# Performance work log

Hardware: AMD Instinct MI355X
Metric: run time of the kernel (lower is better)

Reference implementation:

```python
import jax, jax.numpy as jnp
import numpy as np

HEADS = 2
NEG_SLOPE = 0.2  # PyG GATConv default leaky_relu slope


def gat_conv(x, edge_index, W, a_src, a_dst, bias, num_nodes):
    """PyG-style GATConv with concat=True and self-loops.
    x: [N, Fin], W: [Fin, H*C], a_src/a_dst: [H, C], bias: [H*C].
    edge_index: [2, E] with row 0 = source j, row 1 = target i.
    """
    H = HEADS
    C = W.shape[1] // H
    # add self loops
    loops = jnp.arange(num_nodes, dtype=edge_index.dtype)
    src = jnp.concatenate([edge_index[0], loops])
    dst = jnp.concatenate([edge_index[1], loops])

    xW = (x @ W).reshape(num_nodes, H, C)            # [N, H, C]
    alpha_s = jnp.einsum('nhc,hc->nh', xW, a_src)    # [N, H]
    alpha_d = jnp.einsum('nhc,hc->nh', xW, a_dst)    # [N, H]
    e = alpha_s[src] + alpha_d[dst]                  # [E, H]
    e = jax.nn.leaky_relu(e, NEG_SLOPE)
    # segment softmax over edges sharing the same target node
    m = jax.ops.segment_max(e, dst, num_segments=num_nodes)  # [N, H]
    e = jnp.exp(e - m[dst])
    denom = jax.ops.segment_sum(e, dst, num_segments=num_nodes)  # [N, H]
    alpha = e / denom[dst]                           # [E, H]
    # message = alpha_ij * xW_j, aggregated at target i
    msg = xW[src] * alpha[:, :, None]                # [E, H, C]
    out = jax.ops.segment_sum(msg, dst, num_segments=num_nodes)  # [N, H, C]
    return out.reshape(num_nodes, H * C) + bias


def setup_inputs() -> dict:
    key = jax.random.key(0)
    ks = jax.random.split(key, 10)
    N, E = 50000, 800000
    Fin, D = 128, 128
    H = HEADS
    x = jax.random.normal(ks[0], (N, Fin), dtype=jnp.float32)
    edge_index = jax.random.randint(ks[1], (2, E), 0, N, dtype=jnp.int64)
    g = 1.0 / np.sqrt(Fin)
    W1 = jax.random.normal(ks[2], (Fin, H * D), dtype=jnp.float32) * g
    a_src1 = jax.random.normal(ks[3], (H, D), dtype=jnp.float32) * g
    a_dst1 = jax.random.normal(ks[4], (H, D), dtype=jnp.float32) * g
    b1 = jnp.zeros((H * D,), dtype=jnp.float32)
    g2 = 1.0 / np.sqrt(H * D)
    W2 = jax.random.normal(ks[5], (H * D, H * D), dtype=jnp.float32) * g2
    a_src2 = jax.random.normal(ks[6], (H, D), dtype=jnp.float32) * g2
    a_dst2 = jax.random.normal(ks[7], (H, D), dtype=jnp.float32) * g2
    b2 = jnp.zeros((H * D,), dtype=jnp.float32)
    return {"x": x, "edge_index": edge_index,
            "W1": W1, "a_src1": a_src1, "a_dst1": a_dst1, "b1": b1,
            "W2": W2, "a_src2": a_src2, "a_dst2": a_dst2, "b2": b2}


def reference(x, edge_index, W1, a_src1, a_dst1, b1, W2, a_src2, a_dst2, b2):
    N = x.shape[0]
    h = gat_conv(x, edge_index, W1, a_src1, a_dst1, b1, N)
    h = jax.nn.elu(h)
    # dropout is identity in eval mode (deterministic reference)
    out = gat_conv(h, edge_index, W2, a_src2, a_dst2, b2, N)
    return out
```

## Files before the change

kernel.cpp:

```cpp
#include <hip/hip_runtime.h>
#include <math.h>

#define HEADS 2
#define CH    128
#define HC    256
#define NEG   0.2f

typedef __attribute__((ext_vector_type(8))) _Float16 half8;
typedef __attribute__((ext_vector_type(4))) float    f32x4;

__device__ inline unsigned short f2h(float x) {
    _Float16 h = (_Float16)x;
    unsigned short u;
    __builtin_memcpy(&u, &h, 2);
    return u;
}

__global__ __launch_bounds__(256)
void wcast_kernel(const float* __restrict__ W, unsigned short* __restrict__ Wt, int K) {
    const int idx = blockIdx.x * 256 + threadIdx.x;
    if (idx >= K * HC) return;
    const int k = idx >> 8;
    const int n = idx & 255;
    Wt[(size_t)n * K + k] = f2h(W[idx]);
}

__global__ __launch_bounds__(256)
void va_kernel(const float* __restrict__ W, const float* __restrict__ a_src,
               const float* __restrict__ a_dst, float* __restrict__ va, int K) {
    const int k    = (blockIdx.x * 256 + threadIdx.x) >> 6;
    const int lane = threadIdx.x & 63;
    if (k >= K) return;
    const int c0 = lane * 4;
    const float4 w4 = *reinterpret_cast<const float4*>(&W[(size_t)k * HC + c0]);
    const float4 s4 = *reinterpret_cast<const float4*>(&a_src[c0]);
    const float4 d4 = *reinterpret_cast<const float4*>(&a_dst[c0]);
    float ps = w4.x * s4.x + w4.y * s4.y + w4.z * s4.z + w4.w * s4.w;
    float pd = w4.x * d4.x + w4.y * d4.y + w4.z * d4.z + w4.w * d4.w;
    #pragma unroll
    for (int m = 1; m <= 16; m <<= 1) {
        ps += __shfl_xor(ps, m);
        pd += __shfl_xor(pd, m);
    }
    if (lane == 0)  { va[k * 4 + 0] = ps; va[k * 4 + 2] = pd; }
    if (lane == 32) { va[k * 4 + 1] = ps; va[k * 4 + 3] = pd; }
}

__global__ __launch_bounds__(256)
void xprep_kernel(const float* __restrict__ x, const float* __restrict__ va,
                  unsigned short* __restrict__ xb, float* __restrict__ as_out,
                  float* __restrict__ ad_out, int N, int K) {
    const int i    = (blockIdx.x * 256 + threadIdx.x) >> 6;
    const int lane = threadIdx.x & 63;
    if (i >= N) return;
    const float2 v = reinterpret_cast<const float2*>(&x[(size_t)i * K])[lane];
    ushort2 bv; bv.x = f2h(v.x); bv.y = f2h(v.y);
    reinterpret_cast<ushort2*>(&xb[(size_t)i * K])[lane] = bv;

    const float4 a0 = reinterpret_cast<const float4*>(va)[lane * 2 + 0];
    const float4 a1 = reinterpret_cast<const float4*>(va)[lane * 2 + 1];
    float p0 = v.x * a0.x + v.y * a1.x;
    float p1 = v.x * a0.y + v.y * a1.y;
    float p2 = v.x * a0.z + v.y * a1.z;
    float p3 = v.x * a0.w + v.y * a1.w;
    #pragma unroll
    for (int m = 1; m <= 32; m <<= 1) {
        p0 += __shfl_xor(p0, m);
        p1 += __shfl_xor(p1, m);
        p2 += __shfl_xor(p2, m);
        p3 += __shfl_xor(p3, m);
    }
    if (lane == 0) {
        as_out[i * 2 + 0] = p0; as_out[i * 2 + 1] = p1;
        ad_out[i * 2 + 0] = p2; ad_out[i * 2 + 1] = p3;
    }
}

__global__ __launch_bounds__(256)
void gemm_msg_kernel(const unsigned short* __restrict__ Ab,
                     const unsigned short* __restrict__ Wt,
                     unsigned short* __restrict__ xWh, int M, int K) {
    __shared__ unsigned short Ah[128][40];
    __shared__ unsigned short Bh[128][40];

    const int t    = threadIdx.x;
    const int row0 = blockIdx.x * 128;
    const int col0 = blockIdx.y * 128;
    const int lane = t & 63;
    const int wid  = t >> 6;
    const int wr   = wid >> 1;
    const int wc   = wid & 1;

    f32x4 acc[4][4] = {};

    const int arow = t & 127;
    const int aseg = (t >> 7) * 16;

    for (int kk = 0; kk < K; kk += 32) {
        {
            const int gr = row0 + arow;
            half8 v0 = {0,0,0,0,0,0,0,0}, v1 = {0,0,0,0,0,0,0,0};
            if (gr < M) {
                v0 = *reinterpret_cast<const half8*>(&Ab[(size_t)gr * K + kk + aseg]);
                v1 = *reinterpret_cast<const half8*>(&Ab[(size_t)gr * K + kk + aseg + 8]);
            }
            *reinterpret_cast<half8*>(&Ah[arow][aseg])     = v0;
            *reinterpret_cast<half8*>(&Ah[arow][aseg + 8]) = v1;
            const half8 w0 = *reinterpret_cast<const half8*>(
                &Wt[(size_t)(col0 + arow) * K + kk + aseg]);
            const half8 w1 = *reinterpret_cast<const half8*>(
                &Wt[(size_t)(col0 + arow) * K + kk + aseg + 8]);
            *reinterpret_cast<half8*>(&Bh[arow][aseg])     = w0;
            *reinterpret_cast<half8*>(&Bh[arow][aseg + 8]) = w1;
        }
        __syncthreads();

        half8 ah[4], bh[4];
        const int ko = (lane >> 4) * 8;
        #pragma unroll
        for (int m = 0; m < 4; ++m)
            ah[m] = *reinterpret_cast<const half8*>(&Ah[wr * 64 + m * 16 + (lane & 15)][ko]);
        #pragma unroll
        for (int n = 0; n < 4; ++n)
            bh[n] = *reinterpret_cast<const half8*>(&Bh[wc * 64 + n * 16 + (lane & 15)][ko]);

        #pragma unroll
        for (int m = 0; m < 4; ++m)
            #pragma unroll
            for (int n = 0; n < 4; ++n)
                acc[m][n] = __builtin_amdgcn_mfma_f32_16x16x32_f16(ah[m], bh[n], acc[m][n], 0, 0, 0);
        __syncthreads();
    }

    #pragma unroll
    for (int m = 0; m < 4; ++m) {
        #pragma unroll
        for (int reg = 0; reg < 4; ++reg) {
            const int gr = row0 + wr * 64 + m * 16 + (lane >> 4) * 4 + reg;
            if (gr < M) {
                unsigned short* rp = &xWh[(size_t)gr * HC + col0];
                #pragma unroll
                for (int n = 0; n < 4; ++n)
                    rp[wc * 64 + n * 16 + (lane & 15)] = f2h(acc[m][n][reg]);
            }
        }
    }
}

__global__ __launch_bounds__(256)
void hist_kernel(const int* __restrict__ dst, int* __restrict__ counts, int E) {
    const int e = blockIdx.x * 256 + threadIdx.x;
    if (e < E) atomicAdd(&counts[dst[e]], 1);
}

__global__ __launch_bounds__(256)
void scan_local_kernel(int* __restrict__ data, int* __restrict__ chunk_sum, int N) {
    __shared__ int s[256];
    const int t   = threadIdx.x;
    const int idx = blockIdx.x * 256 + t;
    const int v   = (idx < N) ? data[idx] : 0;
    s[t] = v;
    __syncthreads();
    #pragma unroll
    for (int off = 1; off < 256; off <<= 1) {
        int x = (t >= off) ? s[t - off] : 0;
        __syncthreads();
        s[t] += x;
        __syncthreads();
    }
    if (idx < N) data[idx] = s[t] - v;
    if (t == 255) chunk_sum[blockIdx.x] = s[255];
}

__global__ __launch_bounds__(256)
void scan_chunks_kernel(int* __restrict__ chunk, int nb) {
    __shared__ int s[256];
    const int t = threadIdx.x;
    const int v = (t < nb) ? chunk[t] : 0;
    s[t] = v;
    __syncthreads();
    #pragma unroll
    for (int off = 1; off < 256; off <<= 1) {
        int x = (t >= off) ? s[t - off] : 0;
        __syncthreads();
        s[t] += x;
        __syncthreads();
    }
    if (t < nb) chunk[t] = s[t] - v;
}

__global__ __launch_bounds__(256)
void add_offsets_kernel(const int* __restrict__ excl, const int* __restrict__ chunk_excl,
                        int* __restrict__ row_ptr, int* __restrict__ cursor,
                        int N, int E) {
    const int idx = blockIdx.x * 256 + threadIdx.x;
    if (idx < N) {
        const int rp = excl[idx] + chunk_excl[idx >> 8];
        row_ptr[idx] = rp;
        cursor[idx]  = rp;
    }
    if (idx == 0) row_ptr[N] = E;
}

__global__ __launch_bounds__(256)
void scatter_kernel(const int* __restrict__ src, const int* __restrict__ dst,
                    int* __restrict__ cursor, int* __restrict__ col_idx, int E) {
    const int e = blockIdx.x * 256 + threadIdx.x;
    if (e < E) {
        const int pos = atomicAdd(&cursor[dst[e]], 1);
        col_idx[pos] = src[e];
    }
}

__global__ __launch_bounds__(256)
void agg_kernel(const int* __restrict__ row_ptr, const int* __restrict__ col_idx,
                const unsigned short* __restrict__ xWh,
                const float* __restrict__ as_, const float* __restrict__ ad_,
                const float* __restrict__ bias, float* __restrict__ outf,
                unsigned short* __restrict__ hb, const float* __restrict__ va,
                float* __restrict__ as2, float* __restrict__ ad2,
                int N, int mode) {
    const int wv   = (blockIdx.x * 256 + threadIdx.x) >> 6;
    const int lane = threadIdx.x & 63;
    if (wv >= N) return;
    const int i    = wv;
    const int half = lane >> 5;
    const int sl   = lane & 31;
    const int hh   = sl >> 4;
    const int cb   = hh * 128 + (sl & 15) * 8;
    const float adi = ad_[i * 2 + hh];

    float acc[8] = {};
    float dn = 0.f;

    const int beg = row_ptr[i];
    const int end = row_ptr[i + 1];

    int k = beg + half;
    float asj = 0.f;
    half8 hv = {0,0,0,0,0,0,0,0};
    if (k < end) {
        const int j0 = col_idx[k];
        asj = as_[j0 * 2 + hh];
        hv  = *reinterpret_cast<const half8*>(&xWh[(size_t)j0 * HC + cb]);
    }
    for (; k < end; k += 2) {
        const int kn = k + 2;
        int jn = 0;
        float asn = 0.f;
        half8 hn = {0,0,0,0,0,0,0,0};
        if (kn < end) {
            jn  = col_idx[kn];
            asn = as_[jn * 2 + hh];
            hn  = *reinterpret_cast<const half8*>(&xWh[(size_t)jn * HC + cb]);
        }
        float e = asj + adi;
        e = e > 0.f ? e : NEG * e;
        const float w = __expf(e);
        #pragma unroll
        for (int r = 0; r < 8; ++r)
            acc[r] = fmaf(w, (float)hv[r], acc[r]);
        dn += w;
        hv = hn; asj = asn;
    }

    #pragma unroll
    for (int r = 0; r < 8; ++r) acc[r] += __shfl_xor(acc[r], 32);
    dn += __shfl_xor(dn, 32);

    if (lane < 32) {
        float e = as_[i * 2 + hh] + adi;
        e = e > 0.f ? e : NEG * e;
        const float ws = __expf(e);
        const half8 sv = *reinterpret_cast<const half8*>(&xWh[(size_t)i * HC + cb]);
        #pragma unroll
        for (int r = 0; r < 8; ++r)
            acc[r] = fmaf(ws, (float)sv[r], acc[r]);
        dn += ws;

        const float inv = 1.f / dn;
        const float4 b0 = *reinterpret_cast<const float4*>(&bias[cb]);
        const float4 b1 = *reinterpret_cast<const float4*>(&bias[cb + 4]);
        float o[8];
        o[0] = acc[0] * inv + b0.x; o[1] = acc[1] * inv + b0.y;
        o[2] = acc[2] * inv + b0.z; o[3] = acc[3] * inv + b0.w;
        o[4] = acc[4] * inv + b1.x; o[5] = acc[5] * inv + b1.y;
        o[6] = acc[6] * inv + b1.z; o[7] = acc[7] * inv + b1.w;

        if (mode) {
            #pragma unroll
            for (int r = 0; r < 8; ++r) o[r] = o[r] > 0.f ? o[r] : expm1f(o[r]);
            half8 hvo;
            #pragma unroll
            for (int r = 0; r < 8; ++r) hvo[r] = (_Float16)o[r];
            *reinterpret_cast<half8*>(&hb[(size_t)i * HC + cb]) = hvo;
            float p0 = 0.f, p1 = 0.f, p2 = 0.f, p3 = 0.f;
            #pragma unroll
            for (int r = 0; r < 8; ++r) {
                const float4 vv = reinterpret_cast<const float4*>(va)[cb + r];
                p0 = fmaf(o[r], vv.x, p0);
                p1 = fmaf(o[r], vv.y, p1);
                p2 = fmaf(o[r], vv.z, p2);
                p3 = fmaf(o[r], vv.w, p3);
            }
            #pragma unroll
            for (int m = 1; m <= 16; m <<= 1) {
                p0 += __shfl_xor(p0, m);
                p1 += __shfl_xor(p1, m);
                p2 += __shfl_xor(p2, m);
                p3 += __shfl_xor(p3, m);
            }
            if (sl == 0) {
                as2[i * 2 + 0] = p0; as2[i * 2 + 1] = p1;
                ad2[i * 2 + 0] = p2; ad2[i * 2 + 1] = p3;
            }
        } else {
            *reinterpret_cast<float4*>(&outf[(size_t)i * HC + cb]) =
                make_float4(o[0], o[1], o[2], o[3]);
            *reinterpret_cast<float4*>(&outf[(size_t)i * HC + cb + 4]) =
                make_float4(o[4], o[5], o[6], o[7]);
        }
    }
}

extern "C" void kernel_launch(void* const* d_in, const int* in_sizes, int n_in,
                              void* d_out, int out_size, void* d_ws, size_t ws_size,
                              hipStream_t stream) {
    const float* x      = (const float*)d_in[0];
    const int*   ei     = (const int*)d_in[1];
    const float* W1     = (const float*)d_in[2];
    const float* a_src1 = (const float*)d_in[3];
    const float* a_dst1 = (const float*)d_in[4];
    const float* b1     = (const float*)d_in[5];
    const float* W2     = (const float*)d_in[6];
    const float* a_src2 = (const float*)d_in[7];
    const float* a_dst2 = (const float*)d_in[8];
    const float* b2     = (const float*)d_in[9];
    float* out = (float*)d_out;

    const int Nn = in_sizes[0] / 128;
    const int E  = in_sizes[1] / 2;
    const int K1 = in_sizes[2] / HC;
    const int* src = ei;
    const int* dst = ei + E;

    float* as1   = (float*)d_ws;
    float* ad1   = as1 + (size_t)Nn * 2;
    float* as2   = ad1 + (size_t)Nn * 2;
    float* ad2   = as2 + (size_t)Nn * 2;
    float* va1   = ad2 + (size_t)Nn * 2;
    float* va2   = va1 + (size_t)K1 * 4;
    int*   tmp   = (int*)(va2 + (size_t)HC * 4);
    int*   chunk = tmp + Nn;
    int*   rowp  = chunk + 256;
    int*   curs  = rowp + (Nn + 1);
    int*   colx  = curs + Nn;
    uintptr_t pa = ((uintptr_t)(colx + E) + 31) & ~(uintptr_t)31;
    unsigned short* wt1 = (unsigned short*)pa;
    unsigned short* wt2 = wt1 + (size_t)HC * K1;
    unsigned short* xb  = wt2 + (size_t)HC * HC;
    unsigned short* xWh = xb  + (size_t)Nn * K1;
    unsigned short* hb  = xWh + (size_t)Nn * HC;

    const int nb = (Nn + 255) / 256;

    wcast_kernel<<<(K1 * HC + 255) / 256, 256, 0, stream>>>(W1, wt1, K1);
    wcast_kernel<<<(HC * HC + 255) / 256, 256, 0, stream>>>(W2, wt2, HC);
    va_kernel<<<(K1 + 3) / 4, 256, 0, stream>>>(W1, a_src1, a_dst1, va1, K1);
    va_kernel<<<(HC + 3) / 4, 256, 0, stream>>>(W2, a_src2, a_dst2, va2, HC);
    xprep_kernel<<<(Nn + 3) / 4, 256, 0, stream>>>(x, va1, xb, as1, ad1, Nn, K1);

    hipMemsetAsync(tmp, 0, (size_t)Nn * sizeof(int), stream);
    hist_kernel<<<(E + 255) / 256, 256, 0, stream>>>(dst, tmp, E);
    scan_local_kernel<<<nb, 256, 0, stream>>>(tmp, chunk, Nn);
    scan_chunks_kernel<<<1, 256, 0, stream>>>(chunk, nb);
    add_offsets_kernel<<<nb, 256, 0, stream>>>(tmp, chunk, rowp, curs, Nn, E);
    scatter_kernel<<<(E + 255) / 256, 256, 0, stream>>>(src, dst, curs, colx, E);

    const dim3 ggrid((Nn + 127) / 128, HC / 128);
    const int  agrid = (Nn + 3) / 4;

    gemm_msg_kernel<<<ggrid, 256, 0, stream>>>(xb, wt1, xWh, Nn, K1);
    agg_kernel<<<agrid, 256, 0, stream>>>(rowp, colx, xWh, as1, ad1, b1,
                                          (float*)nullptr, hb, va2, as2, ad2, Nn, 1);

    gemm_msg_kernel<<<ggrid, 256, 0, stream>>>(hb, wt2, xWh, Nn, HC);
    agg_kernel<<<agrid, 256, 0, stream>>>(rowp, colx, xWh, as2, ad2, b2,
                                          out, (unsigned short*)nullptr,
                                          (const float*)nullptr,
                                          (float*)nullptr, (float*)nullptr, Nn, 0);
}
```

Before: 333.9 us.

## Merge prep kernels, deepen GEMM K-tile, and widen aggregation to four edge streams

Merges the two weight-cast launches, the two va launches, and the xprep and histogram kernels into single launches to reduce launch count and idle gaps. The GEMM now stages 64-wide K tiles in shared memory, which halves the number of barrier iterations at the cost of more LDS per block. The aggregation kernel splits each wavefront into four edge streams of 16 lanes, each lane loading 16 channels, so more neighbor gathers are in flight, with an extra shuffle-reduction stage and higher register use.

After: 337.3 us. About the same (+1.0%).

```diff
diff --git a/kernel.cpp b/kernel.cpp
--- a/kernel.cpp
+++ b/kernel.cpp
@@ -17,20 +17,26 @@
 }
 
 __global__ __launch_bounds__(256)
-void wcast_kernel(const float* __restrict__ W, unsigned short* __restrict__ Wt, int K) {
-    const int idx = blockIdx.x * 256 + threadIdx.x;
-    if (idx >= K * HC) return;
-    const int k = idx >> 8;
-    const int n = idx & 255;
-    Wt[(size_t)n * K + k] = f2h(W[idx]);
-}
-
-__global__ __launch_bounds__(256)
-void va_kernel(const float* __restrict__ W, const float* __restrict__ a_src,
-               const float* __restrict__ a_dst, float* __restrict__ va, int K) {
-    const int k    = (blockIdx.x * 256 + threadIdx.x) >> 6;
-    const int lane = threadIdx.x & 63;
-    if (k >= K) return;
+void prep_w_kernel(const float* __restrict__ W1, const float* __restrict__ W2,
+                   unsigned short* __restrict__ wt1, unsigned short* __restrict__ wt2,
+                   int K1) {
+    int idx = blockIdx.x * 256 + threadIdx.x;
+    const int n1 = K1 * HC;
+    if (idx < n1) {
+        const int k = idx >> 8, n = idx & 255;
+        wt1[(size_t)n * K1 + k] = f2h(W1[idx]);
+    } else {
+        idx -= n1;
+        if (idx < HC * HC) {
+            const int k = idx >> 8, n = idx & 255;
+            wt2[(size_t)n * HC + k] = f2h(W2[idx]);
+        }
+    }
+}
+
+__device__ inline void va_row(const float* __restrict__ W, const float* __restrict__ a_src,
+                              const float* __restrict__ a_dst, float* __restrict__ va,
+                              int k, int lane) {
     const int c0 = lane * 4;
     const float4 w4 = *reinterpret_cast<const float4*>(&W[(size_t)k * HC + c0]);
     const float4 s4 = *reinterpret_cast<const float4*>(&a_src[c0]);
@@ -47,9 +53,27 @@
 }
 
 __global__ __launch_bounds__(256)
-void xprep_kernel(const float* __restrict__ x, const float* __restrict__ va,
-                  unsigned short* __restrict__ xb, float* __restrict__ as_out,
-                  float* __restrict__ ad_out, int N, int K) {
+void prep_va_kernel(const float* __restrict__ W1, const float* __restrict__ as1,
+                    const float* __restrict__ ad1, float* __restrict__ va1,
+                    const float* __restrict__ W2, const float* __restrict__ as2,
+                    const float* __restrict__ ad2, float* __restrict__ va2, int K1) {
+    int g = (blockIdx.x * 256 + threadIdx.x) >> 6;
+    const int lane = threadIdx.x & 63;
+    if (g < K1)           va_row(W1, as1, ad1, va1, g, lane);
+    else { g -= K1; if (g < HC) va_row(W2, as2, ad2, va2, g, lane); }
+}
+
+__global__ __launch_bounds__(256)
+void xprep_hist_kernel(const float* __restrict__ x, const float* __restrict__ va,
+                       unsigned short* __restrict__ xb, float* __restrict__ as_out,
+                       float* __restrict__ ad_out, int N, int K,
+                       const int* __restrict__ dst, int* __restrict__ counts,
+                       int E, int nxp) {
+    if ((int)blockIdx.x >= nxp) {
+        const int e = ((int)blockIdx.x - nxp) * 256 + threadIdx.x;
+        if (e < E) atomicAdd(&counts[dst[e]], 1);
+        return;
+    }
     const int i    = (blockIdx.x * 256 + threadIdx.x) >> 6;
     const int lane = threadIdx.x & 63;
     if (i >= N) return;
@@ -80,8 +104,8 @@
 void gemm_msg_kernel(const unsigned short* __restrict__ Ab,
                      const unsigned short* __restrict__ Wt,
                      unsigned short* __restrict__ xWh, int M, int K) {
-    __shared__ unsigned short Ah[128][40];
-    __shared__ unsigned short Bh[128][40];
+    __shared__ unsigned short Ah[128][72];
+    __shared__ unsigned short Bh[128][72];
 
     const int t    = threadIdx.x;
     const int row0 = blockIdx.x * 128;
@@ -94,41 +118,43 @@
     f32x4 acc[4][4] = {};
 
     const int arow = t & 127;
-    const int aseg = (t >> 7) * 16;
-
-    for (int kk = 0; kk < K; kk += 32) {
+    const int aseg = (t >> 7) * 32;
+
+    for (int kk = 0; kk < K; kk += 64) {
         {
             const int gr = row0 + arow;
-            half8 v0 = {0,0,0,0,0,0,0,0}, v1 = {0,0,0,0,0,0,0,0};
-            if (gr < M) {
-                v0 = *reinterpret_cast<const half8*>(&Ab[(size_t)gr * K + kk + aseg]);
-                v1 = *reinterpret_cast<const half8*>(&Ab[(size_t)gr * K + kk + aseg + 8]);
-            }
-            *reinterpret_cast<half8*>(&Ah[arow][aseg])     = v0;
-            *reinterpret_cast<half8*>(&Ah[arow][aseg + 8]) = v1;
-            const half8 w0 = *reinterpret_cast<const half8*>(
-                &Wt[(size_t)(col0 + arow) * K + kk + aseg]);
-            const half8 w1 = *reinterpret_cast<const half8*>(
-                &Wt[(size_t)(col0 + arow) * K + kk + aseg + 8]);
-            *reinterpret_cast<half8*>(&Bh[arow][aseg])     = w0;
-            *reinterpret_cast<half8*>(&Bh[arow][aseg + 8]) = w1;
-        }
-        __syncthreads();
-
-        half8 ah[4], bh[4];
+            #pragma unroll
+            for (int q = 0; q < 4; ++q) {
+                half8 v = {0,0,0,0,0,0,0,0};
+                if (gr < M)
+                    v = *reinterpret_cast<const half8*>(&Ab[(size_t)gr * K + kk + aseg + q * 8]);
+                *reinterpret_cast<half8*>(&Ah[arow][aseg + q * 8]) = v;
+            }
+            #pragma unroll
+            for (int q = 0; q < 4; ++q) {
+                const half8 w = *reinterpret_cast<const half8*>(
+                    &Wt[(size_t)(col0 + arow) * K + kk + aseg + q * 8]);
+                *reinterpret_cast<half8*>(&Bh[arow][aseg + q * 8]) = w;
+            }
+        }
+        __syncthreads();
+
         const int ko = (lane >> 4) * 8;
         #pragma unroll
-        for (int m = 0; m < 4; ++m)
-            ah[m] = *reinterpret_cast<const half8*>(&Ah[wr * 64 + m * 16 + (lane & 15)][ko]);
-        #pragma unroll
-        for (int n = 0; n < 4; ++n)
-            bh[n] = *reinterpret_cast<const half8*>(&Bh[wc * 64 + n * 16 + (lane & 15)][ko]);
-
-        #pragma unroll
-        for (int m = 0; m < 4; ++m)
+        for (int kb = 0; kb < 64; kb += 32) {
+            half8 ah[4], bh[4];
+            #pragma unroll
+            for (int m = 0; m < 4; ++m)
+                ah[m] = *reinterpret_cast<const half8*>(&Ah[wr * 64 + m * 16 + (lane & 15)][kb + ko]);
             #pragma unroll
             for (int n = 0; n < 4; ++n)
-                acc[m][n] = __builtin_amdgcn_mfma_f32_16x16x32_f16(ah[m], bh[n], acc[m][n], 0, 0, 0);
+                bh[n] = *reinterpret_cast<const half8*>(&Bh[wc * 64 + n * 16 + (lane & 15)][kb + ko]);
+            #pragma unroll
+            for (int m = 0; m < 4; ++m)
+                #pragma unroll
+                for (int n = 0; n < 4; ++n)
+                    acc[m][n] = __builtin_amdgcn_mfma_f32_16x16x32_f16(ah[m], bh[n], acc[m][n], 0, 0, 0);
+        }
         __syncthreads();
     }
 
@@ -145,12 +171,6 @@
             }
         }
     }
-}
-
-__global__ __launch_bounds__(256)
-void hist_kernel(const int* __restrict__ dst, int* __restrict__ counts, int E) {
-    const int e = blockIdx.x * 256 + threadIdx.x;
-    if (e < E) atomicAdd(&counts[dst[e]], 1);
 }
 
 __global__ __launch_bounds__(256)
@@ -223,80 +243,96 @@
     const int wv   = (blockIdx.x * 256 + threadIdx.x) >> 6;
     const int lane = threadIdx.x & 63;
     if (wv >= N) return;
-    const int i    = wv;
-    const int half = lane >> 5;
-    const int sl   = lane & 31;
-    const int hh   = sl >> 4;
-    const int cb   = hh * 128 + (sl & 15) * 8;
-    const float adi = ad_[i * 2 + hh];
-
-    float acc[8] = {};
+    const int i      = wv;
+    const int stream = lane >> 4;
+    const int sl     = lane & 15;
+    const int hh     = sl >> 3;
+    const int cb     = sl * 16;
+    const float adi  = ad_[i * 2 + hh];
+
+    float acc[16] = {};
     float dn = 0.f;
 
     const int beg = row_ptr[i];
     const int end = row_ptr[i + 1];
 
-    int k = beg + half;
+    int k = beg + stream;
     float asj = 0.f;
-    half8 hv = {0,0,0,0,0,0,0,0};
+    half8 hv0 = {0,0,0,0,0,0,0,0}, hv1 = {0,0,0,0,0,0,0,0};
     if (k < end) {
         const int j0 = col_idx[k];
         asj = as_[j0 * 2 + hh];
-        hv  = *reinterpret_cast<const half8*>(&xWh[(size_t)j0 * HC + cb]);
-    }
-    for (; k < end; k += 2) {
-        const int kn = k + 2;
-        int jn = 0;
+        hv0 = *reinterpret_cast<const half8*>(&xWh[(size_t)j0 * HC + cb]);
+        hv1 = *reinterpret_cast<const half8*>(&xWh[(size_t)j0 * HC + cb + 8]);
+    }
+    for (; k < end; k += 4) {
+        const int kn = k + 4;
         float asn = 0.f;
-        half8 hn = {0,0,0,0,0,0,0,0};
+        half8 hn0 = {0,0,0,0,0,0,0,0}, hn1 = {0,0,0,0,0,0,0,0};
         if (kn < end) {
-            jn  = col_idx[kn];
+            const int jn = col_idx[kn];
             asn = as_[jn * 2 + hh];
-            hn  = *reinterpret_cast<const half8*>(&xWh[(size_t)jn * HC + cb]);
+            hn0 = *reinterpret_cast<const half8*>(&xWh[(size_t)jn * HC + cb]);
+            hn1 = *reinterpret_cast<const half8*>(&xWh[(size_t)jn * HC + cb + 8]);
         }
         float e = asj + adi;
         e = e > 0.f ? e : NEG * e;
         const float w = __expf(e);
         #pragma unroll
-        for (int r = 0; r < 8; ++r)
-            acc[r] = fmaf(w, (float)hv[r], acc[r]);
+        for (int r = 0; r < 8; ++r) {
+            acc[r]     = fmaf(w, (float)hv0[r], acc[r]);
+            acc[r + 8] = fmaf(w, (float)hv1[r], acc[r + 8]);
+        }
         dn += w;
-        hv = hn; asj = asn;
-    }
-
-    #pragma unroll
-    for (int r = 0; r < 8; ++r) acc[r] += __shfl_xor(acc[r], 32);
+        hv0 = hn0; hv1 = hn1; asj = asn;
+    }
+
+    #pragma unroll
+    for (int r = 0; r < 16; ++r) {
+        acc[r] += __shfl_xor(acc[r], 16);
+        acc[r] += __shfl_xor(acc[r], 32);
+    }
+    dn += __shfl_xor(dn, 16);
     dn += __shfl_xor(dn, 32);
 
-    if (lane < 32) {
+    if (lane < 16) {
         float e = as_[i * 2 + hh] + adi;
         e = e > 0.f ? e : NEG * e;
         const float ws = __expf(e);
-        const half8 sv = *reinterpret_cast<const half8*>(&xWh[(size_t)i * HC + cb]);
+        const half8 s0 = *reinterpret_cast<const half8*>(&xWh[(size_t)i * HC + cb]);
+        const half8 s1 = *reinterpret_cast<const half8*>(&xWh[(size_t)i * HC + cb + 8]);
         #pragma unroll
-        for (int r = 0; r < 8; ++r)
-            acc[r] = fmaf(ws, (float)sv[r], acc[r]);
+        for (int r = 0; r < 8; ++r) {
+            acc[r]     = fmaf(ws, (float)s0[r], acc[r]);
+            acc[r + 8] = fmaf(ws, (float)s1[r], acc[r + 8]);
+        }
         dn += ws;
 
         const float inv = 1.f / dn;
-        const float4 b0 = *reinterpret_cast<const float4*>(&bias[cb]);
-        const float4 b1 = *reinterpret_cast<const float4*>(&bias[cb + 4]);
-        float o[8];
-        o[0] = acc[0] * inv + b0.x; o[1] = acc[1] * inv + b0.y;
-        o[2] = acc[2] * inv + b0.z; o[3] = acc[3] * inv + b0.w;
-        o[4] = acc[4] * inv + b1.x; o[5] = acc[5] * inv + b1.y;
-        o[6] = acc[6] * inv + b1.z; o[7] = acc[7] * inv + b1.w;
+        float o[16];
+        #pragma unroll
+        for (int r = 0; r < 4; ++r) {
+            const float4 b4 = *reinterpret_cast<const float4*>(&bias[cb + r * 4]);
+            o[r * 4 + 0] = acc[r * 4 + 0] * inv + b4.x;
+            o[r * 4 + 1] = acc[r * 4 + 1] * inv + b4.y;
+            o[r * 4 + 2] = acc[r * 4 + 2] * inv + b4.z;
+            o[r * 4 + 3] = acc[r * 4 + 3] * inv + b4.w;
+        }
 
         if (mode) {
             #pragma unroll
-            for (int r = 0; r < 8; ++r) o[r] = o[r] > 0.f ? o[r] : expm1f(o[r]);
-            half8 hvo;
-            #pragma unroll
-            for (int r = 0; r < 8; ++r) hvo[r] = (_Float16)o[r];
-            *reinterpret_cast<half8*>(&hb[(size_t)i * HC + cb]) = hvo;
+            for (int r = 0; r < 16; ++r) o[r] = o[r] > 0.f ? o[r] : expm1f(o[r]);
+            half8 ho0, ho1;
+            #pragma unroll
+            for (int r = 0; r < 8; ++r) {
+                ho0[r] = (_Float16)o[r];
+                ho1[r] = (_Float16)o[r + 8];
+            }
+            *reinterpret_cast<half8*>(&hb[(size_t)i * HC + cb])     = ho0;
+            *reinterpret_cast<half8*>(&hb[(size_t)i * HC + cb + 8]) = ho1;
             float p0 = 0.f, p1 = 0.f, p2 = 0.f, p3 = 0.f;
             #pragma unroll
-            for (int r = 0; r < 8; ++r) {
+            for (int r = 0; r < 16; ++r) {
                 const float4 vv = reinterpret_cast<const float4*>(va)[cb + r];
                 p0 = fmaf(o[r], vv.x, p0);
                 p1 = fmaf(o[r], vv.y, p1);
@@ -304,7 +340,7 @@
                 p3 = fmaf(o[r], vv.w, p3);
             }
             #pragma unroll
-            for (int m = 1; m <= 16; m <<= 1) {
+            for (int m = 1; m <= 8; m <<= 1) {
                 p0 += __shfl_xor(p0, m);
                 p1 += __shfl_xor(p1, m);
                 p2 += __shfl_xor(p2, m);
@@ -315,10 +351,10 @@
                 ad2[i * 2 + 0] = p2; ad2[i * 2 + 1] = p3;
             }
         } else {
-            *reinterpret_cast<float4*>(&outf[(size_t)i * HC + cb]) =
-                make_float4(o[0], o[1], o[2], o[3]);
-            *reinterpret_cast<float4*>(&outf[(size_t)i * HC + cb + 4]) =
-                make_float4(o[4], o[5], o[6], o[7]);
+            #pragma unroll
+            for (int r = 0; r < 4; ++r)
+                *reinterpret_cast<float4*>(&outf[(size_t)i * HC + cb + r * 4]) =
+                    make_float4(o[r * 4 + 0], o[r * 4 + 1], o[r * 4 + 2], o[r * 4 + 3]);
         }
     }
 }
@@ -362,20 +398,20 @@
     unsigned short* xWh = xb  + (size_t)Nn * K1;
     unsigned short* hb  = xWh + (size_t)Nn * HC;
 
-    const int nb = (Nn + 255) / 256;
-
-    wcast_kernel<<<(K1 * HC + 255) / 256, 256, 0, stream>>>(W1, wt1, K1);
-    wcast_kernel<<<(HC * HC + 255) / 256, 256, 0, stream>>>(W2, wt2, HC);
-    va_kernel<<<(K1 + 3) / 4, 256, 0, stream>>>(W1, a_src1, a_dst1, va1, K1);
-    va_kernel<<<(HC + 3) / 4, 256, 0, stream>>>(W2, a_src2, a_dst2, va2, HC);
-    xprep_kernel<<<(Nn + 3) / 4, 256, 0, stream>>>(x, va1, xb, as1, ad1, Nn, K1);
+    const int nb  = (Nn + 255) / 256;
+    const int nxp = (Nn + 3) / 4;
+    const int nhb = (E + 255) / 256;
 
     hipMemsetAsync(tmp, 0, (size_t)Nn * sizeof(int), stream);
-    hist_kernel<<<(E + 255) / 256, 256, 0, stream>>>(dst, tmp, E);
+    prep_w_kernel<<<(K1 * HC + HC * HC + 255) / 256, 256, 0, stream>>>(W1, W2, wt1, wt2, K1);
+    prep_va_kernel<<<(K1 + HC + 3) / 4, 256, 0, stream>>>(W1, a_src1, a_dst1, va1,
+                                                          W2, a_src2, a_dst2, va2, K1);
+    xprep_hist_kernel<<<nxp + nhb, 256, 0, stream>>>(x, va1, xb, as1, ad1, Nn, K1,
+                                                     dst, tmp, E, nxp);
     scan_local_kernel<<<nb, 256, 0, stream>>>(tmp, chunk, Nn);
     scan_chunks_kernel<<<1, 256, 0, stream>>>(chunk, nb);
     add_offsets_kernel<<<nb, 256, 0, stream>>>(tmp, chunk, rowp, curs, Nn, E);
-    scatter_kernel<<<(E + 255) / 256, 256, 0, stream>>>(src, dst, curs, colx, E);
+    scatter_kernel<<<nhb, 256, 0, stream>>>(src, dst, curs, colx, E);
 
     const dim3 ggrid((Nn + 127) / 128, HC / 128);
     const int  agrid = (Nn + 3) / 4;
```
